# Performance work log

Measured on AMD Instinct MI355X. Metric: run time of the kernel, lower is better.

## Reference

```python
import jax, jax.numpy as jnp
import numpy as np

EMB, H, KV, HD = 2048, 32, 8, 64
G = H // KV  # group size = 4
SEQ, B = 2048, 1
EPS = 1e-6


def rms_norm(x, scale):
    # fp32 RMSNorm over last dim, no bias/centering
    v = jnp.mean(x.astype(jnp.float32) ** 2, axis=-1, keepdims=True)
    return (x * jax.lax.rsqrt(v + EPS) * scale).astype(x.dtype)


def apply_rope(x, cos, sin):
    # x: [b, h, s, d]; cos/sin: [s, d]
    d2 = x.shape[-1] // 2
    x1, x2 = x[..., :d2], x[..., d2:]
    rot = jnp.concatenate((-x2, x1), axis=-1)
    return (x * cos[None, None] + rot * sin[None, None]).astype(x.dtype)


def setup_inputs() -> dict:
    key = jax.random.key(0)
    ks = jax.random.split(key, 6)
    x = jax.random.normal(ks[0], (B, SEQ, EMB), jnp.float32)
    mask = jnp.triu(jnp.ones((SEQ, SEQ), jnp.bool_), k=1)  # causal: True = masked
    inv_freq = 1.0 / (10000.0 ** (np.arange(0, HD, 2, dtype=np.float32) / HD))
    t = np.arange(SEQ, dtype=np.float32)
    ang = np.outer(t, inv_freq)  # [seq, hd/2]
    ang = np.concatenate([ang, ang], axis=-1)  # [seq, hd]
    cos = jnp.asarray(np.cos(ang), jnp.float32)
    sin = jnp.asarray(np.sin(ang), jnp.float32)
    s = 0.02
    Wq = jax.random.normal(ks[1], (EMB, H * HD), jnp.float32) * s
    Wk = jax.random.normal(ks[2], (EMB, KV * HD), jnp.float32) * s
    Wv = jax.random.normal(ks[3], (EMB, KV * HD), jnp.float32) * s
    Wo = jax.random.normal(ks[4], (H * HD, EMB), jnp.float32) * s
    q_scale = jnp.ones((HD,), jnp.float32)
    k_scale = jnp.ones((HD,), jnp.float32)
    return {"x": x, "mask": mask, "cos": cos, "sin": sin, "Wq": Wq, "Wk": Wk,
            "Wv": Wv, "Wo": Wo, "q_scale": q_scale, "k_scale": k_scale}


def reference(x, mask, cos, sin, Wq, Wk, Wv, Wo, q_scale, k_scale):
    b, s, _ = x.shape
    q = (x @ Wq).reshape(b, s, H, HD).transpose(0, 2, 1, 3)     # [b,h,s,d]
    k = (x @ Wk).reshape(b, s, KV, HD).transpose(0, 2, 1, 3)    # [b,kv,s,d]
    v = (x @ Wv).reshape(b, s, KV, HD).transpose(0, 2, 1, 3)
    q = rms_norm(q, q_scale)
    k = rms_norm(k, k_scale)
    q = apply_rope(q, cos, sin)
    k = apply_rope(k, cos, sin)
    # grouped heads: h = kv*G + g (matches repeat_interleave along head dim)
    qg = q.reshape(b, KV, G, s, HD)
    scores = jnp.einsum('bkgqd,bkld->bkgql', qg, k) / jnp.sqrt(jnp.float32(HD))
    scores = jnp.where(mask[None, None, None], -jnp.inf, scores)
    w = jax.nn.softmax(scores.astype(jnp.float32), axis=-1).astype(q.dtype)
    ctx = jnp.einsum('bkgql,bkld->bkgqd', w, v)                 # [b,kv,g,s,d]
    ctx = ctx.reshape(b, H, s, HD).transpose(0, 2, 1, 3).reshape(b, s, H * HD)
    return ctx @ Wo
```

## Files before the change

### kernel.cpp

```cpp
#include <hip/hip_runtime.h>
#include <stdint.h>

#define EMB 2048
#define NH 32
#define NKV 8
#define HD 64
#define SEQ 2048
#define QKV_N 3072

using u16 = unsigned short;
typedef __attribute__((ext_vector_type(8))) short bf16x8;
typedef __attribute__((ext_vector_type(4))) float f32x4;
typedef __attribute__((ext_vector_type(4))) unsigned short u16x4;

#define MFMA16(a, b, c) __builtin_amdgcn_mfma_f32_16x16x32_bf16(a, b, c, 0, 0, 0)

__device__ inline u16 f2b(float f) {
  union { float f; unsigned u; } v; v.f = f;
  unsigned r = v.u + 0x7fffu + ((v.u >> 16) & 1u);
  return (u16)(r >> 16);
}

__device__ inline void gload16(const void* g, void* l) {
  __builtin_amdgcn_global_load_lds(
      (const __attribute__((address_space(1))) void*)g,
      (__attribute__((address_space(3))) void*)l, 16, 0, 0);
}

__global__ void cvt_x(const float* __restrict__ x, u16* __restrict__ xb) {
  int i = blockIdx.x * blockDim.x + threadIdx.x;
  float4 v = ((const float4*)x)[i];
  u16x4 o = { f2b(v.x), f2b(v.y), f2b(v.z), f2b(v.w) };
  ((u16x4*)xb)[i] = o;
}

__global__ void wtrans(const float* __restrict__ src, u16* __restrict__ dst, int R, int C) {
  __shared__ float t[64][65];
  int tx = threadIdx.x & 63, ty = threadIdx.x >> 6;
  int r0 = blockIdx.y * 64, c0 = blockIdx.x * 64;
#pragma unroll
  for (int i = 0; i < 16; ++i) {
    int r = ty * 16 + i;
    t[r][tx] = src[(size_t)(r0 + r) * C + c0 + tx];
  }
  __syncthreads();
#pragma unroll
  for (int i = 0; i < 16; ++i) {
    int r = ty * 16 + i;
    dst[(size_t)(c0 + r) * R + r0 + tx] = f2b(t[tx][r]);
  }
}

__global__ void wtrans_qkv(const float* __restrict__ Wq, const float* __restrict__ Wk,
                           const float* __restrict__ Wv, u16* __restrict__ dst) {
  __shared__ float t[64][65];
  int tx = threadIdx.x & 63, ty = threadIdx.x >> 6;
  int bx = blockIdx.x;
  int r0 = blockIdx.y * 64;
  const float* src; int C, c0;
  if (bx < 32)      { src = Wq; C = 2048; c0 = bx * 64; }
  else if (bx < 40) { src = Wk; C = 512;  c0 = (bx - 32) * 64; }
  else              { src = Wv; C = 512;  c0 = (bx - 40) * 64; }
#pragma unroll
  for (int i = 0; i < 16; ++i) {
    int r = ty * 16 + i;
    t[r][tx] = src[(size_t)(r0 + r) * C + c0 + tx];
  }
  __syncthreads();
  int drow = bx * 64;
#pragma unroll
  for (int i = 0; i < 16; ++i) {
    int r = ty * 16 + i;
    dst[(size_t)(drow + r) * 2048 + r0 + tx] = f2b(t[tx][r]);
  }
}

template<int OUT_MODE>
__global__ __launch_bounds__(256, 2)
void gemm_bt(const u16* __restrict__ A, const u16* __restrict__ BT,
             float* __restrict__ Cp, int M, int N, int K, int nwgy,
             const float* __restrict__ cosT, const float* __restrict__ sinT,
             const float* __restrict__ qsc, const float* __restrict__ ksc,
             u16* __restrict__ qb, u16* __restrict__ kb, u16* __restrict__ vT) {
  __shared__ u16 As[2][64 * 64];
  __shared__ u16 Bs[2][128 * 64];
  const int tid = threadIdx.x;
  const int w = tid >> 6, lane = tid & 63;
  const int lr = lane & 15, lg = lane >> 4;
  const int nwg = gridDim.x, cpx = nwg >> 3, pos = blockIdx.x;
  const int o = (pos & 7) * cpx + (pos >> 3);
  const int by = o % nwgy, bx = o / nwgy;
  const int m0 = by * 64, n0 = bx * 128;
  const int wm = (w >> 1) * 32, wn = (w & 1) * 64;
  f32x4 acc[2][4] = {};
  const int nk = K >> 6;

  auto STAGE = [&](int buf, int kt) {
    const int k0 = kt << 6;
    const int j = tid & 7;
    const int rr = tid >> 3;
#pragma unroll
    for (int i = 0; i < 2; ++i) {
      int r = i * 32 + rr;
      int sc = (j ^ (r & 7)) * 8;
      gload16(&A[(size_t)(m0 + r) * K + k0 + sc], (char*)As[buf] + i * 4096 + w * 1024);
    }
#pragma unroll
    for (int i = 0; i < 4; ++i) {
      int r = i * 32 + rr;
      int sc = (j ^ (r & 7)) * 8;
      gload16(&BT[(size_t)(n0 + r) * K + k0 + sc], (char*)Bs[buf] + i * 4096 + w * 1024);
    }
  };

  int cur = 0;
  STAGE(0, 0);
  asm volatile("s_waitcnt vmcnt(0)" ::: "memory");
  __syncthreads();
  for (int kt = 0; kt < nk; ++kt) {
    if (kt + 1 < nk) STAGE(cur ^ 1, kt + 1);
#pragma unroll
    for (int ks = 0; ks < 2; ++ks) {
      bf16x8 a[2], b[4];
#pragma unroll
      for (int i = 0; i < 2; ++i) {
        int row = wm + i * 16 + lr;
        a[i] = *(const bf16x8*)&As[cur][row * 64 + ((ks * 4 + lg) ^ (row & 7)) * 8];
      }
#pragma unroll
      for (int j = 0; j < 4; ++j) {
        int row = wn + j * 16 + lr;
        b[j] = *(const bf16x8*)&Bs[cur][row * 64 + ((ks * 4 + lg) ^ (row & 7)) * 8];
      }
#pragma unroll
      for (int i = 0; i < 2; ++i)
#pragma unroll
        for (int j = 0; j < 4; ++j)
          acc[i][j] = MFMA16(a[i], b[j], acc[i][j]);
    }
    asm volatile("s_waitcnt vmcnt(0)" ::: "memory");
    __syncthreads();
    cur ^= 1;
  }

  if (OUT_MODE == 0) {
#pragma unroll
    for (int i = 0; i < 2; ++i)
#pragma unroll
      for (int j = 0; j < 4; ++j)
#pragma unroll
        for (int r = 0; r < 4; ++r) {
          int row = m0 + wm + i * 16 + lg * 4 + r;
          int col = n0 + wn + j * 16 + lr;
          Cp[(size_t)row * N + col] = acc[i][j][r];
        }
  } else {
    const int hh = (n0 + wn) >> 6;
    if (hh < 40) {
      const float* scp = (hh < 32) ? qsc : ksc;
      u16* dst = (hh < 32) ? (qb + (size_t)hh * SEQ * HD)
                           : (kb + (size_t)(hh - 32) * SEQ * HD);
      const float qmul = (hh < 32) ? 0.125f : 1.0f;
#pragma unroll
      for (int i = 0; i < 2; ++i)
#pragma unroll
        for (int r = 0; r < 4; ++r) {
          float ssq = 0.f;
#pragma unroll
          for (int j = 0; j < 4; ++j) ssq += acc[i][j][r] * acc[i][j][r];
          ssq += __shfl_xor(ssq, 1);
          ssq += __shfl_xor(ssq, 2);
          ssq += __shfl_xor(ssq, 4);
          ssq += __shfl_xor(ssq, 8);
          float rs = rsqrtf(ssq * (1.0f / 64.0f) + 1e-6f);
          int s = m0 + wm + i * 16 + lg * 4 + r;
          float xn[4];
#pragma unroll
          for (int j = 0; j < 4; ++j) xn[j] = acc[i][j][r] * rs * scp[j * 16 + lr];
#pragma unroll
          for (int j = 0; j < 2; ++j) {
            int d = j * 16 + lr;
            float o1 = (xn[j] * cosT[s * 64 + d] - xn[j + 2] * sinT[s * 64 + d]) * qmul;
            float o2 = (xn[j + 2] * cosT[s * 64 + 32 + d] + xn[j] * sinT[s * 64 + 32 + d]) * qmul;
            dst[(size_t)s * 64 + d] = f2b(o1);
            dst[(size_t)s * 64 + 32 + d] = f2b(o2);
          }
        }
    } else {
      const int kvh = hh - 40;
      const int sbase = m0 + wm + lg * 4;
#pragma unroll
      for (int i = 0; i < 2; ++i)
#pragma unroll
        for (int j = 0; j < 4; ++j) {
          int d = j * 16 + lr;
          u16x4 pk = { f2b(acc[i][j][0]), f2b(acc[i][j][1]),
                       f2b(acc[i][j][2]), f2b(acc[i][j][3]) };
          *(u16x4*)&vT[((size_t)kvh * HD + d) * SEQ + sbase + i * 16] = pk;
        }
    }
  }
}

template<bool MASKED>
__device__ __forceinline__ void attn_step(
    const u16* __restrict__ Ks, const u16* __restrict__ VTs, u16* __restrict__ Psw,
    bf16x8 q0, bf16x8 q1, f32x4* O, float* l_acc,
    int qbase, int kbase, int lr, int lg) {
  f32x4 sc[4];
#pragma unroll
  for (int kj = 0; kj < 4; ++kj) {
    int r2 = kj * 16 + lr, sw = r2 & 7;
    bf16x8 kf0 = *(const bf16x8*)&Ks[r2 * 64 + (lg ^ sw) * 8];
    bf16x8 kf1 = *(const bf16x8*)&Ks[r2 * 64 + ((4 + lg) ^ sw) * 8];
    f32x4 z = {};
    z = MFMA16(q0, kf0, z);
    z = MFMA16(q1, kf1, z);
    sc[kj] = z;
  }
#pragma unroll
  for (int kj = 0; kj < 4; ++kj)
#pragma unroll
    for (int r = 0; r < 4; ++r) {
      float p;
      if (MASKED) {
        int qg = qbase + lg * 4 + r;
        int kg = kbase + kj * 16 + lr;
        p = (kg > qg) ? 0.0f : __expf(sc[kj][r] - 8.0f);
      } else {
        p = __expf(sc[kj][r] - 8.0f);
      }
      l_acc[r] += p;
      int row = lg * 4 + r, col = kj * 16 + lr;
      int sj = (col >> 3) ^ (row & 7);
      Psw[row * 64 + sj * 8 + (col & 7)] = f2b(p);
    }
#pragma unroll
  for (int ks2 = 0; ks2 < 2; ++ks2) {
    bf16x8 pa = *(const bf16x8*)&Psw[lr * 64 + ((ks2 * 4 + lg) ^ (lr & 7)) * 8];
#pragma unroll
    for (int n = 0; n < 4; ++n) {
      int r3 = n * 16 + lr, sw3 = r3 & 7;
      bf16x8 vb = *(const bf16x8*)&VTs[r3 * 64 + ((ks2 * 4 + lg) ^ sw3) * 8];
      O[n] = MFMA16(pa, vb, O[n]);
    }
  }
}

__global__ __launch_bounds__(256, 2)
void attn(const u16* __restrict__ qb, const u16* __restrict__ kb,
          const u16* __restrict__ vT, u16* __restrict__ ctx) {
  __shared__ u16 Ks[2][64 * 64];
  __shared__ u16 VTs[2][64 * 64];
  __shared__ u16 Ps[4][16 * 64];
  const int tid = threadIdx.x, w = tid >> 6, lane = tid & 63;
  const int lr = lane & 15, lg = lane >> 4;
  const int pos = blockIdx.x;
  const int o = (pos & 7) * 64 + (pos >> 3);
  const int h = o >> 4, p = o & 15;
  const int kvh = h >> 2;
  const int qtA = p, qtB = 31 - p;
  const int qbaseA = qtA * 64 + w * 16, qbaseB = qtB * 64 + w * 16;
  u16* Psw = &Ps[w][0];

  bf16x8 qA0 = *(const bf16x8*)&qb[((size_t)h * SEQ + qbaseA + lr) * HD + lg * 8];
  bf16x8 qA1 = *(const bf16x8*)&qb[((size_t)h * SEQ + qbaseA + lr) * HD + 32 + lg * 8];
  bf16x8 qB0 = *(const bf16x8*)&qb[((size_t)h * SEQ + qbaseB + lr) * HD + lg * 8];
  bf16x8 qB1 = *(const bf16x8*)&qb[((size_t)h * SEQ + qbaseB + lr) * HD + 32 + lg * 8];

  f32x4 OA[4] = {}, OB[4] = {};
  float lA[4] = {0.f, 0.f, 0.f, 0.f}, lB[4] = {0.f, 0.f, 0.f, 0.f};

  auto STAGE = [&](int buf, int kt) {
    const int kbase = kt * 64;
#pragma unroll
    for (int i = 0; i < 2; ++i) {
      int c = i * 256 + tid;
      int r = c >> 3, j = c & 7, sj = j ^ (r & 7);
      gload16(&kb[((size_t)kvh * SEQ + kbase + r) * HD + sj * 8],
              (char*)Ks[buf] + i * 4096 + w * 1024);
      gload16(&vT[((size_t)kvh * HD + r) * SEQ + kbase + sj * 8],
              (char*)VTs[buf] + i * 4096 + w * 1024);
    }
  };

  int cur = 0;
  STAGE(0, 0);
  asm volatile("s_waitcnt vmcnt(0)" ::: "memory");
  __syncthreads();
  for (int kt = 0; kt <= qtB; ++kt) {
    if (kt < qtB) STAGE(cur ^ 1, kt + 1);
    const int kbase = kt * 64;
    if (kt <= qtA) {
      if (kt == qtA)
        attn_step<true >(Ks[cur], VTs[cur], Psw, qA0, qA1, OA, lA, qbaseA, kbase, lr, lg);
      else
        attn_step<false>(Ks[cur], VTs[cur], Psw, qA0, qA1, OA, lA, qbaseA, kbase, lr, lg);
    }
    if (kt == qtB)
      attn_step<true >(Ks[cur], VTs[cur], Psw, qB0, qB1, OB, lB, qbaseB, kbase, lr, lg);
    else
      attn_step<false>(Ks[cur], VTs[cur], Psw, qB0, qB1, OB, lB, qbaseB, kbase, lr, lg);
    asm volatile("s_waitcnt vmcnt(0)" ::: "memory");
    __syncthreads();
    cur ^= 1;
  }

#pragma unroll
  for (int r = 0; r < 4; ++r) {
#pragma unroll
    for (int off = 1; off < 16; off <<= 1) {
      lA[r] += __shfl_xor(lA[r], off);
      lB[r] += __shfl_xor(lB[r], off);
    }
  }
#pragma unroll
  for (int n = 0; n < 4; ++n)
#pragma unroll
    for (int r = 0; r < 4; ++r) {
      int sA = qbaseA + lg * 4 + r;
      ctx[(size_t)sA * 2048 + h * 64 + n * 16 + lr] = f2b(OA[n][r] / lA[r]);
      int sB = qbaseB + lg * 4 + r;
      ctx[(size_t)sB * 2048 + h * 64 + n * 16 + lr] = f2b(OB[n][r] / lB[r]);
    }
}

extern "C" void kernel_launch(void* const* d_in, const int* in_sizes, int n_in,
                              void* d_out, int out_size, void* d_ws, size_t ws_size,
                              hipStream_t stream) {
  const float* x    = (const float*)d_in[0];
  const float* cosT = (const float*)d_in[2];
  const float* sinT = (const float*)d_in[3];
  const float* Wq   = (const float*)d_in[4];
  const float* Wk   = (const float*)d_in[5];
  const float* Wv   = (const float*)d_in[6];
  const float* Wo   = (const float*)d_in[7];
  const float* qsc  = (const float*)d_in[8];
  const float* ksc  = (const float*)d_in[9];
  float* out = (float*)d_out;

  char* wsp = (char*)d_ws;
  u16*   xb    = (u16*)(wsp);
  u16*   WqkvT = (u16*)(wsp + ((size_t)8  << 20));
  u16*   WoT   = (u16*)(wsp + ((size_t)20 << 20));
  u16*   qbuf  = (u16*)(wsp + ((size_t)28 << 20));
  u16*   kbuf  = (u16*)(wsp + ((size_t)36 << 20));
  u16*   vTbuf = (u16*)(wsp + ((size_t)38 << 20));
  u16*   ctxb  = (u16*)(wsp + ((size_t)40 << 20));

  cvt_x<<<4096, 256, 0, stream>>>(x, xb);
  wtrans_qkv<<<dim3(48, 32), 256, 0, stream>>>(Wq, Wk, Wv, WqkvT);
  wtrans<<<dim3(32, 32), 256, 0, stream>>>(Wo, WoT, 2048, 2048);

  gemm_bt<2><<<768, 256, 0, stream>>>(xb, WqkvT, nullptr, 2048, 3072, 2048, 32,
                                      cosT, sinT, qsc, ksc, qbuf, kbuf, vTbuf);
  attn<<<512, 256, 0, stream>>>(qbuf, kbuf, vTbuf, ctxb);
  gemm_bt<0><<<512, 256, 0, stream>>>((const u16*)ctxb, WoT, out, 2048, 2048, 2048, 32,
                                      nullptr, nullptr, nullptr, nullptr,
                                      nullptr, nullptr, nullptr);
}
```

Before: 128.5 us.

## Split paired causal query tiles into separate blocks and use exp2 softmax

```diff
diff --git a/kernel.cpp b/kernel.cpp
--- a/kernel.cpp
+++ b/kernel.cpp
@@ -14,11 +14,16 @@
 typedef __attribute__((ext_vector_type(4))) unsigned short u16x4;
 
 #define MFMA16(a, b, c) __builtin_amdgcn_mfma_f32_16x16x32_bf16(a, b, c, 0, 0, 0)
+#define EXP2_C8 11.5415603f
 
 __device__ inline u16 f2b(float f) {
   union { float f; unsigned u; } v; v.f = f;
   unsigned r = v.u + 0x7fffu + ((v.u >> 16) & 1u);
   return (u16)(r >> 16);
+}
+__device__ inline u16 f2b_fast(float f) {
+  union { float f; unsigned u; } v; v.f = f;
+  return (u16)((v.u + 0x8000u) >> 16);
 }
 
 __device__ inline void gload16(const void* g, void* l) {
@@ -160,7 +165,7 @@
       const float* scp = (hh < 32) ? qsc : ksc;
       u16* dst = (hh < 32) ? (qb + (size_t)hh * SEQ * HD)
                            : (kb + (size_t)(hh - 32) * SEQ * HD);
-      const float qmul = (hh < 32) ? 0.125f : 1.0f;
+      const float qmul = (hh < 32) ? 0.18033688f : 1.0f;
 #pragma unroll
       for (int i = 0; i < 2; ++i)
 #pragma unroll
@@ -226,14 +231,14 @@
       if (MASKED) {
         int qg = qbase + lg * 4 + r;
         int kg = kbase + kj * 16 + lr;
-        p = (kg > qg) ? 0.0f : __expf(sc[kj][r] - 8.0f);
+        p = (kg > qg) ? 0.0f : exp2f(sc[kj][r] - EXP2_C8);
       } else {
-        p = __expf(sc[kj][r] - 8.0f);
+        p = exp2f(sc[kj][r] - EXP2_C8);
       }
       l_acc[r] += p;
       int row = lg * 4 + r, col = kj * 16 + lr;
       int sj = (col >> 3) ^ (row & 7);
-      Psw[row * 64 + sj * 8 + (col & 7)] = f2b(p);
+      Psw[row * 64 + sj * 8 + (col & 7)] = f2b_fast(p);
     }
 #pragma unroll
   for (int ks2 = 0; ks2 < 2; ++ks2) {
@@ -256,20 +261,17 @@
   const int tid = threadIdx.x, w = tid >> 6, lane = tid & 63;
   const int lr = lane & 15, lg = lane >> 4;
   const int pos = blockIdx.x;
-  const int o = (pos & 7) * 64 + (pos >> 3);
-  const int h = o >> 4, p = o & 15;
+  const int o = (pos & 7) * 128 + (pos >> 3);
+  const int h = o >> 5, qt = 31 - (o & 31);
   const int kvh = h >> 2;
-  const int qtA = p, qtB = 31 - p;
-  const int qbaseA = qtA * 64 + w * 16, qbaseB = qtB * 64 + w * 16;
+  const int qbase = qt * 64 + w * 16;
   u16* Psw = &Ps[w][0];
 
-  bf16x8 qA0 = *(const bf16x8*)&qb[((size_t)h * SEQ + qbaseA + lr) * HD + lg * 8];
-  bf16x8 qA1 = *(const bf16x8*)&qb[((size_t)h * SEQ + qbaseA + lr) * HD + 32 + lg * 8];
-  bf16x8 qB0 = *(const bf16x8*)&qb[((size_t)h * SEQ + qbaseB + lr) * HD + lg * 8];
-  bf16x8 qB1 = *(const bf16x8*)&qb[((size_t)h * SEQ + qbaseB + lr) * HD + 32 + lg * 8];
-
-  f32x4 OA[4] = {}, OB[4] = {};
-  float lA[4] = {0.f, 0.f, 0.f, 0.f}, lB[4] = {0.f, 0.f, 0.f, 0.f};
+  bf16x8 q0 = *(const bf16x8*)&qb[((size_t)h * SEQ + qbase + lr) * HD + lg * 8];
+  bf16x8 q1 = *(const bf16x8*)&qb[((size_t)h * SEQ + qbase + lr) * HD + 32 + lg * 8];
+
+  f32x4 O[4] = {};
+  float l_acc[4] = {0.f, 0.f, 0.f, 0.f};
 
   auto STAGE = [&](int buf, int kt) {
     const int kbase = kt * 64;
@@ -288,40 +290,29 @@
   STAGE(0, 0);
   asm volatile("s_waitcnt vmcnt(0)" ::: "memory");
   __syncthreads();
-  for (int kt = 0; kt <= qtB; ++kt) {
-    if (kt < qtB) STAGE(cur ^ 1, kt + 1);
+  for (int kt = 0; kt <= qt; ++kt) {
+    if (kt < qt) STAGE(cur ^ 1, kt + 1);
     const int kbase = kt * 64;
-    if (kt <= qtA) {
-      if (kt == qtA)
-        attn_step<true >(Ks[cur], VTs[cur], Psw, qA0, qA1, OA, lA, qbaseA, kbase, lr, lg);
-      else
-        attn_step<false>(Ks[cur], VTs[cur], Psw, qA0, qA1, OA, lA, qbaseA, kbase, lr, lg);
-    }
-    if (kt == qtB)
-      attn_step<true >(Ks[cur], VTs[cur], Psw, qB0, qB1, OB, lB, qbaseB, kbase, lr, lg);
+    if (kt == qt)
+      attn_step<true >(Ks[cur], VTs[cur], Psw, q0, q1, O, l_acc, qbase, kbase, lr, lg);
     else
-      attn_step<false>(Ks[cur], VTs[cur], Psw, qB0, qB1, OB, lB, qbaseB, kbase, lr, lg);
+      attn_step<false>(Ks[cur], VTs[cur], Psw, q0, q1, O, l_acc, qbase, kbase, lr, lg);
     asm volatile("s_waitcnt vmcnt(0)" ::: "memory");
     __syncthreads();
     cur ^= 1;
   }
 
 #pragma unroll
-  for (int r = 0; r < 4; ++r) {
-#pragma unroll
-    for (int off = 1; off < 16; off <<= 1) {
-      lA[r] += __shfl_xor(lA[r], off);
-      lB[r] += __shfl_xor(lB[r], off);
-    }
-  }
+  for (int r = 0; r < 4; ++r)
+#pragma unroll
+    for (int off = 1; off < 16; off <<= 1)
+      l_acc[r] += __shfl_xor(l_acc[r], off);
 #pragma unroll
   for (int n = 0; n < 4; ++n)
 #pragma unroll
     for (int r = 0; r < 4; ++r) {
-      int sA = qbaseA + lg * 4 + r;
-      ctx[(size_t)sA * 2048 + h * 64 + n * 16 + lr] = f2b(OA[n][r] / lA[r]);
-      int sB = qbaseB + lg * 4 + r;
-      ctx[(size_t)sB * 2048 + h * 64 + n * 16 + lr] = f2b(OB[n][r] / lB[r]);
+      int s = qbase + lg * 4 + r;
+      ctx[(size_t)s * 2048 + h * 64 + n * 16 + lr] = f2b(O[n][r] / l_acc[r]);
     }
 }
 
@@ -354,7 +345,7 @@
 
   gemm_bt<2><<<768, 256, 0, stream>>>(xb, WqkvT, nullptr, 2048, 3072, 2048, 32,
                                       cosT, sinT, qsc, ksc, qbuf, kbuf, vTbuf);
-  attn<<<512, 256, 0, stream>>>(qbuf, kbuf, vTbuf, ctxb);
+  attn<<<1024, 256, 0, stream>>>(qbuf, kbuf, vTbuf, ctxb);
   gemm_bt<0><<<512, 256, 0, stream>>>((const u16*)ctxb, WoT, out, 2048, 2048, 2048, 32,
                                       nullptr, nullptr, nullptr, nullptr,
                                       nullptr, nullptr, nullptr);
```

Measured after the change: 154.0 us. 19.8% more time.

## Keep attention probabilities in registers via transposed QK MFMA and lane shuffles

Applied to the files above, without the earlier changes.

```diff
diff --git a/kernel.cpp b/kernel.cpp
--- a/kernel.cpp
+++ b/kernel.cpp
@@ -14,11 +14,18 @@
 typedef __attribute__((ext_vector_type(4))) unsigned short u16x4;
 
 #define MFMA16(a, b, c) __builtin_amdgcn_mfma_f32_16x16x32_bf16(a, b, c, 0, 0, 0)
+#define EXP2_C8 11.5415603f
 
 __device__ inline u16 f2b(float f) {
   union { float f; unsigned u; } v; v.f = f;
   unsigned r = v.u + 0x7fffu + ((v.u >> 16) & 1u);
   return (u16)(r >> 16);
+}
+
+__device__ inline unsigned cvt_pk_bf16(float lo, float hi) {
+  unsigned d;
+  asm("v_cvt_pk_bf16_f32 %0, %1, %2" : "=v"(d) : "v"(lo), "v"(hi));
+  return d;
 }
 
 __device__ inline void gload16(const void* g, void* l) {
@@ -160,7 +167,7 @@
       const float* scp = (hh < 32) ? qsc : ksc;
       u16* dst = (hh < 32) ? (qb + (size_t)hh * SEQ * HD)
                            : (kb + (size_t)(hh - 32) * SEQ * HD);
-      const float qmul = (hh < 32) ? 0.125f : 1.0f;
+      const float qmul = (hh < 32) ? 0.18033688f : 1.0f;
 #pragma unroll
       for (int i = 0; i < 2; ++i)
 #pragma unroll
@@ -204,46 +211,66 @@
 
 template<bool MASKED>
 __device__ __forceinline__ void attn_step(
-    const u16* __restrict__ Ks, const u16* __restrict__ VTs, u16* __restrict__ Psw,
-    bf16x8 q0, bf16x8 q1, f32x4* O, float* l_acc,
+    const u16* __restrict__ Ks, const u16* __restrict__ VTs,
+    bf16x8 q0, bf16x8 q1, f32x4* O, float& l_acc,
     int qbase, int kbase, int lr, int lg) {
   f32x4 sc[4];
+  __builtin_amdgcn_s_setprio(1);
 #pragma unroll
   for (int kj = 0; kj < 4; ++kj) {
     int r2 = kj * 16 + lr, sw = r2 & 7;
     bf16x8 kf0 = *(const bf16x8*)&Ks[r2 * 64 + (lg ^ sw) * 8];
     bf16x8 kf1 = *(const bf16x8*)&Ks[r2 * 64 + ((4 + lg) ^ sw) * 8];
     f32x4 z = {};
-    z = MFMA16(q0, kf0, z);
-    z = MFMA16(q1, kf1, z);
+    z = MFMA16(kf0, q0, z);
+    z = MFMA16(kf1, q1, z);
     sc[kj] = z;
   }
-#pragma unroll
-  for (int kj = 0; kj < 4; ++kj)
+  __builtin_amdgcn_s_setprio(0);
+  unsigned wpk[4][2];
+  const int qg = qbase + lr;
+#pragma unroll
+  for (int kj = 0; kj < 4; ++kj) {
+    float p[4];
 #pragma unroll
     for (int r = 0; r < 4; ++r) {
-      float p;
       if (MASKED) {
-        int qg = qbase + lg * 4 + r;
-        int kg = kbase + kj * 16 + lr;
-        p = (kg > qg) ? 0.0f : __expf(sc[kj][r] - 8.0f);
+        int kg = kbase + kj * 16 + lg * 4 + r;
+        p[r] = (kg > qg) ? 0.0f : exp2f(sc[kj][r] - EXP2_C8);
       } else {
-        p = __expf(sc[kj][r] - 8.0f);
+        p[r] = exp2f(sc[kj][r] - EXP2_C8);
       }
-      l_acc[r] += p;
-      int row = lg * 4 + r, col = kj * 16 + lr;
-      int sj = (col >> 3) ^ (row & 7);
-      Psw[row * 64 + sj * 8 + (col & 7)] = f2b(p);
-    }
+    }
+    l_acc += (p[0] + p[1]) + (p[2] + p[3]);
+    wpk[kj][0] = cvt_pk_bf16(p[0], p[1]);
+    wpk[kj][1] = cvt_pk_bf16(p[2], p[3]);
+  }
+  const int s0 = lr + ((lg & 1) << 5);
+  const int s1 = s0 + 16;
+  const bool hi = (lg >> 1) & 1;
 #pragma unroll
   for (int ks2 = 0; ks2 < 2; ++ks2) {
-    bf16x8 pa = *(const bf16x8*)&Psw[lr * 64 + ((ks2 * 4 + lg) ^ (lr & 7)) * 8];
+    unsigned a0 = (unsigned)__shfl((int)wpk[ks2 * 2][0], s0);
+    unsigned a1 = (unsigned)__shfl((int)wpk[ks2 * 2][1], s0);
+    unsigned b0 = (unsigned)__shfl((int)wpk[ks2 * 2 + 1][0], s0);
+    unsigned b1 = (unsigned)__shfl((int)wpk[ks2 * 2 + 1][1], s0);
+    unsigned c0 = (unsigned)__shfl((int)wpk[ks2 * 2][0], s1);
+    unsigned c1 = (unsigned)__shfl((int)wpk[ks2 * 2][1], s1);
+    unsigned d0 = (unsigned)__shfl((int)wpk[ks2 * 2 + 1][0], s1);
+    unsigned d1 = (unsigned)__shfl((int)wpk[ks2 * 2 + 1][1], s1);
+    union { unsigned u[4]; bf16x8 v; } pa;
+    pa.u[0] = hi ? b0 : a0;
+    pa.u[1] = hi ? b1 : a1;
+    pa.u[2] = hi ? d0 : c0;
+    pa.u[3] = hi ? d1 : c1;
+    __builtin_amdgcn_s_setprio(1);
 #pragma unroll
     for (int n = 0; n < 4; ++n) {
       int r3 = n * 16 + lr, sw3 = r3 & 7;
       bf16x8 vb = *(const bf16x8*)&VTs[r3 * 64 + ((ks2 * 4 + lg) ^ sw3) * 8];
-      O[n] = MFMA16(pa, vb, O[n]);
-    }
+      O[n] = MFMA16(pa.v, vb, O[n]);
+    }
+    __builtin_amdgcn_s_setprio(0);
   }
 }
 
@@ -252,7 +279,6 @@
           const u16* __restrict__ vT, u16* __restrict__ ctx) {
   __shared__ u16 Ks[2][64 * 64];
   __shared__ u16 VTs[2][64 * 64];
-  __shared__ u16 Ps[4][16 * 64];
   const int tid = threadIdx.x, w = tid >> 6, lane = tid & 63;
   const int lr = lane & 15, lg = lane >> 4;
   const int pos = blockIdx.x;
@@ -261,7 +287,6 @@
   const int kvh = h >> 2;
   const int qtA = p, qtB = 31 - p;
   const int qbaseA = qtA * 64 + w * 16, qbaseB = qtB * 64 + w * 16;
-  u16* Psw = &Ps[w][0];
 
   bf16x8 qA0 = *(const bf16x8*)&qb[((size_t)h * SEQ + qbaseA + lr) * HD + lg * 8];
   bf16x8 qA1 = *(const bf16x8*)&qb[((size_t)h * SEQ + qbaseA + lr) * HD + 32 + lg * 8];
@@ -269,7 +294,7 @@
   bf16x8 qB1 = *(const bf16x8*)&qb[((size_t)h * SEQ + qbaseB + lr) * HD + 32 + lg * 8];
 
   f32x4 OA[4] = {}, OB[4] = {};
-  float lA[4] = {0.f, 0.f, 0.f, 0.f}, lB[4] = {0.f, 0.f, 0.f, 0.f};
+  float lA = 0.f, lB = 0.f;
 
   auto STAGE = [&](int buf, int kt) {
     const int kbase = kt * 64;
@@ -293,35 +318,35 @@
     const int kbase = kt * 64;
     if (kt <= qtA) {
       if (kt == qtA)
-        attn_step<true >(Ks[cur], VTs[cur], Psw, qA0, qA1, OA, lA, qbaseA, kbase, lr, lg);
+        attn_step<true >(Ks[cur], VTs[cur], qA0, qA1, OA, lA, qbaseA, kbase, lr, lg);
       else
-        attn_step<false>(Ks[cur], VTs[cur], Psw, qA0, qA1, OA, lA, qbaseA, kbase, lr, lg);
+        attn_step<false>(Ks[cur], VTs[cur], qA0, qA1, OA, lA, qbaseA, kbase, lr, lg);
     }
     if (kt == qtB)
-      attn_step<true >(Ks[cur], VTs[cur], Psw, qB0, qB1, OB, lB, qbaseB, kbase, lr, lg);
+      attn_step<true >(Ks[cur], VTs[cur], qB0, qB1, OB, lB, qbaseB, kbase, lr, lg);
     else
-      attn_step<false>(Ks[cur], VTs[cur], Psw, qB0, qB1, OB, lB, qbaseB, kbase, lr, lg);
+      attn_step<false>(Ks[cur], VTs[cur], qB0, qB1, OB, lB, qbaseB, kbase, lr, lg);
     asm volatile("s_waitcnt vmcnt(0)" ::: "memory");
     __syncthreads();
     cur ^= 1;
   }
 
+  lA += __shfl_xor(lA, 16); lA += __shfl_xor(lA, 32);
+  lB += __shfl_xor(lB, 16); lB += __shfl_xor(lB, 32);
+  float lAr[4], lBr[4];
 #pragma unroll
   for (int r = 0; r < 4; ++r) {
-#pragma unroll
-    for (int off = 1; off < 16; off <<= 1) {
-      lA[r] += __shfl_xor(lA[r], off);
-      lB[r] += __shfl_xor(lB[r], off);
-    }
+    lAr[r] = __shfl(lA, lg * 4 + r);
+    lBr[r] = __shfl(lB, lg * 4 + r);
   }
 #pragma unroll
   for (int n = 0; n < 4; ++n)
 #pragma unroll
     for (int r = 0; r < 4; ++r) {
       int sA = qbaseA + lg * 4 + r;
-      ctx[(size_t)sA * 2048 + h * 64 + n * 16 + lr] = f2b(OA[n][r] / lA[r]);
+      ctx[(size_t)sA * 2048 + h * 64 + n * 16 + lr] = f2b(OA[n][r] / lAr[r]);
       int sB = qbaseB + lg * 4 + r;
-      ctx[(size_t)sB * 2048 + h * 64 + n * 16 + lr] = f2b(OB[n][r] / lB[r]);
+      ctx[(size_t)sB * 2048 + h * 64 + n * 16 + lr] = f2b(OB[n][r] / lBr[r]);
     }
 }
 
```

After: 134.8 us. 1.05x slower.
